# Kernel tuning notes

Measured on AMD Instinct MI355X. Metric: run time of the kernel, lower is better.

## Reference

```python
import jax, jax.numpy as jnp
import numpy as np

NUM_NODES = 16384
NUM_EDGES = 131072
NUM_MOLS = 512
H = 256          # hidden_dim
L = 3            # num_hidden_layers
NUM_RBF = 50
CUTOFF = 5.0
IN_DIM = 5
D_IN = IN_DIM + 3  # atom_types + spherical coords


def setup_inputs() -> dict:
    ks = jax.random.split(jax.random.key(0), 32)
    n = lambda k, s: jax.random.normal(k, s, dtype=jnp.float32) * 0.05
    return {
        "atom_types": jax.random.uniform(ks[0], (NUM_NODES, IN_DIM), dtype=jnp.float32),
        "coords_spherical": jax.random.normal(ks[1], (NUM_NODES, 3), dtype=jnp.float32),
        "edge_dist": jax.random.uniform(ks[2], (NUM_EDGES,), dtype=jnp.float32) * CUTOFF,
        "edge_index": jax.random.randint(ks[3], (2, NUM_EDGES), 0, NUM_NODES, dtype=jnp.int32),
        "node2mol": jnp.arange(NUM_NODES, dtype=jnp.int32) // (NUM_NODES // NUM_MOLS),
        "emb_Wm": n(ks[4], (D_IN, H)), "emb_bm": jnp.zeros((H,), jnp.float32),
        "emb_Wp": n(ks[5], (D_IN, H)), "emb_bp": jnp.zeros((H,), jnp.float32),
        "attn_Wqm": n(ks[6], (L, H, H)), "attn_Wkm": n(ks[7], (L, H, H)), "attn_Wvm": n(ks[8], (L, H, H)),
        "attn_Wqp": n(ks[9], (L, H, H)), "attn_Wkp": n(ks[10], (L, H, H)), "attn_Wvp": n(ks[11], (L, H, H)),
        "attn_We": n(ks[12], (L, NUM_RBF)), "attn_be": jnp.zeros((L,), jnp.float32),
        "mp_We": n(ks[13], (L, NUM_RBF, H)), "mp_be": jnp.zeros((L, H), jnp.float32),
        "mp_Wm": n(ks[14], (L, H, H)), "mp_bm": jnp.zeros((L, H), jnp.float32),
        "mp_Wp": n(ks[15], (L, H, H)), "mp_bp": jnp.zeros((L, H), jnp.float32),
        "ln_g": jnp.ones((L, H), jnp.float32), "ln_b": jnp.zeros((L, H), jnp.float32),
        "proj_W": n(ks[16], (H, H)), "proj_b": jnp.zeros((H,), jnp.float32),
        "head_W1": n(ks[17], (2 * H, H)), "head_b1": jnp.zeros((H,), jnp.float32),
        "head_W2": n(ks[18], (H, H // 2)), "head_b2": jnp.zeros((H // 2,), jnp.float32),
        "head_W3": n(ks[19], (H // 2, 1)), "head_b3": jnp.zeros((1,), jnp.float32),
    }


def _seg_softmax(s, seg, n):
    m = jax.ops.segment_max(s, seg, num_segments=n)
    e = jnp.exp(s - m[seg])
    z = jax.ops.segment_sum(e, seg, num_segments=n)
    return e / (z[seg] + 1e-9)


def _layernorm(x, g, b):
    mu = x.mean(-1, keepdims=True)
    v = ((x - mu) ** 2).mean(-1, keepdims=True)
    return (x - mu) * jax.lax.rsqrt(v + 1e-5) * g + b


def _forward(atom_types, coords_spherical, edge_dist,
             emb_Wm, emb_bm, emb_Wp, emb_bp,
             attn_Wqm, attn_Wkm, attn_Wvm, attn_Wqp, attn_Wkp, attn_Wvp, attn_We, attn_be,
             mp_We, mp_be, mp_Wm, mp_bm, mp_Wp, mp_bp,
             ln_g, ln_b, proj_W, proj_b,
             head_W1, head_b1, head_W2, head_b2, head_W3, head_b3,
             edge_index, node2mol):
    src, dst = edge_index[0], edge_index[1]
    N = NUM_NODES

    # --- RBF expansion (Schutt 2018): 50 gaussians on [0, cutoff] * cosine cutoff ---
    centers = jnp.linspace(0.0, CUTOFF, NUM_RBF)
    delta = CUTOFF / NUM_RBF
    env = 0.5 * (jnp.cos(jnp.pi * edge_dist / CUTOFF) + 1.0) * (edge_dist < CUTOFF)
    rbf = jnp.exp(-0.5 * ((edge_dist[:, None] - centers) / delta) ** 2) * env[:, None]  # [E, R]

    # --- Complex polar embedding ---
    x = jnp.concatenate([atom_types, coords_spherical], axis=-1)  # [N, 8]
    mag = jax.nn.softplus(x @ emb_Wm + emb_bm)
    ph = jnp.pi * jnp.tanh(x @ emb_Wp + emb_bp)

    for l in range(L):
        # --- Complex polar attention: |q||k| cos(phi_q - phi_k), edge bias from rbf ---
        qm, km, vm = mag @ attn_Wqm[l], mag @ attn_Wkm[l], mag @ attn_Wvm[l]
        qp, kp, vp = ph @ attn_Wqp[l], ph @ attn_Wkp[l], ph @ attn_Wvp[l]
        score = jnp.sum(qm[dst] * km[src] * jnp.cos(qp[dst] - kp[src]), axis=-1) / jnp.sqrt(float(H))
        score = score + rbf @ attn_We[l] + attn_be[l]          # [E]
        alpha = _seg_softmax(score, dst, N)                    # [E]
        new_mag = jax.ops.segment_sum(alpha[:, None] * vm[src], dst, num_segments=N)
        new_ph = jax.ops.segment_sum(alpha[:, None] * vp[src], dst, num_segments=N)

        # --- Complex message passing gated by RBF profile ---
        gate = jax.nn.silu(rbf @ mp_We[l] + mp_be[l])          # [E, H]
        agg_m = jax.ops.segment_sum(gate * new_mag[src], dst, num_segments=N)
        agg_p = jax.ops.segment_sum(gate * new_ph[src], dst, num_segments=N)
        new_mag = new_mag + agg_m @ mp_Wm[l] + mp_bm[l]
        new_ph = new_ph + agg_p @ mp_Wp[l] + mp_bp[l]

        # --- residual + LayerNorm on magnitude (dropout = identity at eval) ---
        new_mag = new_mag + mag
        new_ph = new_ph + ph
        mag = _layernorm(new_mag, ln_g[l], ln_b[l])
        ph = new_ph

    # --- real projection + dual (mean, sum) pooling per molecule ---
    atom_repr = (mag * jnp.cos(ph)) @ proj_W + proj_b          # [N, H]
    s = jax.ops.segment_sum(atom_repr, node2mol, num_segments=NUM_MOLS)
    cnt = jax.ops.segment_sum(jnp.ones((N, 1), atom_repr.dtype), node2mol, num_segments=NUM_MOLS)
    mol = jnp.concatenate([s / jnp.maximum(cnt, 1.0), s], axis=-1)  # [B, 2H]

    h = jax.nn.silu(mol @ head_W1 + head_b1)
    h = jax.nn.silu(h @ head_W2 + head_b2)
    return h @ head_W3 + head_b3                               # [B, 1]


def reference(atom_types, coords_spherical, edge_dist,
              emb_Wm, emb_bm, emb_Wp, emb_bp,
              attn_Wqm, attn_Wkm, attn_Wvm, attn_Wqp, attn_Wkp, attn_Wvp, attn_We, attn_be,
              mp_We, mp_be, mp_Wm, mp_bm, mp_Wp, mp_bp,
              ln_g, ln_b, proj_W, proj_b,
              head_W1, head_b1, head_W2, head_b2, head_W3, head_b3,
              edge_index, node2mol):
    return _forward(atom_types, coords_spherical, edge_dist,
                    emb_Wm, emb_bm, emb_Wp, emb_bp,
                    attn_Wqm, attn_Wkm, attn_Wvm, attn_Wqp, attn_Wkp, attn_Wvp, attn_We, attn_be,
                    mp_We, mp_be, mp_Wm, mp_bm, mp_Wp, mp_bp,
                    ln_g, ln_b, proj_W, proj_b,
                    head_W1, head_b1, head_W2, head_b2, head_W3, head_b3,
                    edge_index, node2mol)
```

## Files before the change

kernel.cpp:

```cpp
#include <hip/hip_runtime.h>
#include <math.h>

#define N_NODES 16384
#define N_EDGES 131072
#define N_MOLS 512
#define HDIM 256
#define NLAYER 3
#define NRBF 50
#define CUT 5.0f
#define HH (HDIM*HDIM)

typedef unsigned short u16;
typedef __attribute__((ext_vector_type(8))) short short8v;
typedef __attribute__((ext_vector_type(4))) float f32x4;
typedef __attribute__((ext_vector_type(4))) unsigned short u16x4;
typedef __attribute__((ext_vector_type(8))) unsigned short u16x8;
typedef __attribute__((ext_vector_type(2))) unsigned short u16x2;

__device__ __forceinline__ float softplusf(float x){ return fmaxf(x,0.f)+log1pf(expf(-fabsf(x))); }
__device__ __forceinline__ float siluf(float x){ return x/(1.f+expf(-x)); }
__device__ __forceinline__ float bf2f(u16 u){ union{unsigned int i; float f;}v; v.i=((unsigned int)u)<<16; return v.f; }
__device__ __forceinline__ u16 f2bf(float f){ union{float f; unsigned int i;}v; v.f=f; unsigned int r = v.i + 0x7FFFu + ((v.i>>16)&1u); return (u16)(r>>16); }

__device__ __forceinline__ void gload_lds16(const void* g, void* l){
  __builtin_amdgcn_global_load_lds((const __attribute__((address_space(1))) unsigned int*)g,
                                   (__attribute__((address_space(3))) unsigned int*)l, 16, 0, 0);
}

__global__ void k_hist(const int* __restrict__ dst, int* __restrict__ cnt){
  int e = blockIdx.x*256 + threadIdx.x;
  if(e < N_EDGES) atomicAdd(&cnt[dst[e]], 1);
}

__global__ __launch_bounds__(1024) void k_scan(const int* __restrict__ cnt,
                                               int* __restrict__ rowptr,
                                               int* __restrict__ cursor){
  __shared__ int part[1024];
  int tid = threadIdx.x;
  int base = tid*16;
  int loc[16]; int s=0;
  #pragma unroll
  for(int i=0;i<16;i++){ loc[i]=s; s+=cnt[base+i]; }
  part[tid]=s; __syncthreads();
  for(int off=1; off<1024; off<<=1){
    int v = (tid>=off)? part[tid-off] : 0;
    __syncthreads();
    part[tid] += v;
    __syncthreads();
  }
  int pre = (tid==0)?0:part[tid-1];
  #pragma unroll
  for(int i=0;i<16;i++){ int v = pre+loc[i]; rowptr[base+i]=v; cursor[base+i]=v; }
  if(tid==1023) rowptr[N_NODES]=part[1023];
}

__global__ void k_scatter(const int* __restrict__ dst, const int* __restrict__ src,
                          int* __restrict__ cursor,
                          int* __restrict__ perm, int* __restrict__ srcp){
  int e = blockIdx.x*256+threadIdx.x;
  if(e<N_EDGES){
    int p = atomicAdd(&cursor[dst[e]],1);
    perm[p]=e;
    srcp[p]=src[e];
  }
}

__global__ void k_rbf(const float* __restrict__ dist, const int* __restrict__ perm,
                      u16* __restrict__ rbfp){
  int gid = blockIdx.x*256+threadIdx.x;
  int i = gid>>6, r = gid&63;
  int e = perm[i];
  u16 o = 0;
  if(r<NRBF){
    float d = dist[e];
    float env = 0.5f*(cosf(3.14159265358979f*d/CUT)+1.f) * (d<CUT ? 1.f:0.f);
    float c = CUT*(float)r/(float)(NRBF-1);
    float u = (d - c)/(CUT/(float)NRBF);
    o = f2bf(expf(-0.5f*u*u)*env);
  }
  rbfp[(size_t)i*64+r] = o;
}

struct WDesc { const float* src; u16* dst; int K; int dK; };
struct WArgs { WDesc d[28]; };
__global__ __launch_bounds__(256) void k_wconv(WArgs a){
  WDesc w = a.d[blockIdx.x];
  int t = blockIdx.y;
  int ky = t >> 3, nx = t & 7;
  if(ky*32 >= w.dK) return;
  __shared__ float tile[32][33];
  int tid = threadIdx.x;
  int kk = tid >> 3, n4 = (tid & 7)*4;
  int k = ky*32 + kk;
  float4 v = {0.f,0.f,0.f,0.f};
  if(k < w.K) v = *(const float4*)(w.src + (size_t)k*HDIM + nx*32 + n4);
  tile[kk][n4+0]=v.x; tile[kk][n4+1]=v.y; tile[kk][n4+2]=v.z; tile[kk][n4+3]=v.w;
  __syncthreads();
  int nn = tid >> 3, k4 = (tid & 7)*4;
  u16x4 o;
  #pragma unroll
  for(int j=0;j<4;j++) o[j] = f2bf(tile[k4+j][nn]);
  *(u16x4*)(w.dst + (size_t)(nx*32+nn)*w.dK + ky*32 + k4) = o;
}

__global__ void k_embed(const float* __restrict__ at, const float* __restrict__ co,
                        const float* __restrict__ Wm, const float* __restrict__ bm,
                        const float* __restrict__ Wp, const float* __restrict__ bp,
                        float* __restrict__ mag, float* __restrict__ ph,
                        u16* __restrict__ magb, u16* __restrict__ phb){
  int n = blockIdx.x; int h = threadIdx.x;
  __shared__ float x[8];
  if(threadIdx.x<5) x[threadIdx.x] = at[n*5+threadIdx.x];
  else if(threadIdx.x<8) x[threadIdx.x] = co[n*3+threadIdx.x-5];
  __syncthreads();
  float tm=bm[h], tp=bp[h];
  #pragma unroll
  for(int i=0;i<8;i++){ tm = fmaf(x[i],Wm[i*HDIM+h],tm); tp = fmaf(x[i],Wp[i*HDIM+h],tp); }
  size_t idx = (size_t)n*HDIM+h;
  float m = softplusf(tm);
  float p = 3.14159265358979f*tanhf(tp);
  mag[idx]=m; ph[idx]=p; magb[idx]=f2bf(m); phb[idx]=f2bf(p);
}

template<int MODE>
__device__ __forceinline__ void gemm_fullN(const u16* __restrict__ A,
                                           const u16* __restrict__ Bt,
                                           const float* __restrict__ bias,
                                           void* __restrict__ outp, int K){
  __shared__ __align__(16) u16 As[128*64];
  __shared__ __align__(16) u16 Bs[256*64];
  int tid = threadIdx.x;
  int lane = tid & 63, wid = tid >> 6;
  int wm = wid & 1, wn = wid >> 1;
  int m0 = blockIdx.y * 128;
  const size_t Kb = (size_t)K*2;
  f32x4 acc[4][4] = {};
  for(int k0=0;k0<K;k0+=64){
    #pragma unroll
    for(int it=0; it<2; it++){
      int ci = it*512 + tid;
      int row = ci>>3, cl = ci&7;
      int csw = cl ^ (row&7);
      size_t go = (size_t)(m0+row)*Kb + (size_t)k0*2 + csw*16;
      gload_lds16((const char*)A+go, (char*)As + it*8192 + wid*1024);
    }
    #pragma unroll
    for(int it=0; it<4; it++){
      int ci = it*512 + tid;
      int row = ci>>3, cl = ci&7;
      int csw = cl ^ (row&7);
      size_t go = (size_t)row*Kb + (size_t)k0*2 + csw*16;
      gload_lds16((const char*)Bt+go, (char*)Bs + it*8192 + wid*1024);
    }
    __syncthreads();
    #pragma unroll
    for(int ks=0;ks<2;ks++){
      short8v a[4], b[4];
      #pragma unroll
      for(int fm=0;fm<4;fm++){
        int m = wm*64 + fm*16 + (lane&15);
        int ch = (ks*4 + (lane>>4)) ^ (m&7);
        a[fm] = *(const short8v*)&As[m*64 + ch*8];
      }
      #pragma unroll
      for(int fn=0;fn<4;fn++){
        int n = wn*64 + fn*16 + (lane&15);
        int ch = (ks*4 + (lane>>4)) ^ (n&7);
        b[fn] = *(const short8v*)&Bs[n*64 + ch*8];
      }
      #pragma unroll
      for(int fm=0;fm<4;fm++)
        #pragma unroll
        for(int fn=0;fn<4;fn++)
          acc[fm][fn] = __builtin_amdgcn_mfma_f32_16x16x32_bf16(a[fm], b[fn], acc[fm][fn],0,0,0);
    }
    __syncthreads();
  }
  int ro=(lane>>4)*4, co=lane&15;
  #pragma unroll
  for(int fm=0;fm<4;fm++){
    #pragma unroll
    for(int fn=0;fn<4;fn++){
      int col = wn*64 + fn*16 + co;
      float bv = bias ? bias[col] : 0.f;
      #pragma unroll
      for(int r=0;r<4;r++){
        int row = m0 + wm*64 + fm*16 + ro + r;
        float v = acc[fm][fn][r] + bv;
        size_t ci = (size_t)row*256 + col;
        if(MODE==1) ((u16*)outp)[ci] = f2bf(siluf(v));
        else if(MODE==2) ((float*)outp)[ci] += v;
        else ((float*)outp)[ci] = v;
      }
    }
  }
}

__global__ __launch_bounds__(512) void k_gemm_gate(const u16* __restrict__ rbfp,
                                                   const u16* __restrict__ Wt,
                                                   const float* __restrict__ be,
                                                   u16* __restrict__ gate){
  gemm_fullN<1>(rbfp, Wt, be, gate, 64);
}
struct MpArgs { const u16* A[2]; const u16* Wt[2]; const float* b[2]; float* C[2]; };
__global__ __launch_bounds__(512) void k_gemm_mp(MpArgs a){
  int z = blockIdx.z;
  gemm_fullN<2>(a.A[z], a.Wt[z], a.b[z], a.C[z], HDIM);
}
__global__ __launch_bounds__(512) void k_gemm_proj(const u16* __restrict__ Ab,
                                                   const u16* __restrict__ Wt,
                                                   const float* __restrict__ b,
                                                   float* __restrict__ C){
  gemm_fullN<3>(Ab, Wt, b, C, HDIM);
}

struct Qkv3Args { const u16* Wm[3]; const u16* Wp[3]; u16* qpk; u16* kvpk; };
__global__ __launch_bounds__(512) void k_gemm_qkv3(const u16* __restrict__ magb,
                                                   const u16* __restrict__ phb,
                                                   Qkv3Args a){
  __shared__ __align__(16) u16 Ams[128*64];
  __shared__ __align__(16) u16 Aps[128*64];
  __shared__ __align__(16) u16 Bms[256*64];
  __shared__ __align__(16) u16 Bps[256*64];
  int z = blockIdx.z;
  const u16* Wmz = a.Wm[z];
  const u16* Wpz = a.Wp[z];
  int tid = threadIdx.x;
  int lane = tid & 63, wid = tid >> 6;
  int wm = wid & 1, wn = wid >> 1;
  int m0 = blockIdx.y * 128;
  const size_t Kb = 512;
  f32x4 accm[4][4] = {}, accp[4][4] = {};
  for(int k0=0;k0<256;k0+=64){
    #pragma unroll
    for(int it=0; it<2; it++){
      int ci = it*512 + tid;
      int row = ci>>3, cl = ci&7;
      int csw = cl ^ (row&7);
      size_t go = (size_t)(m0+row)*Kb + (size_t)k0*2 + csw*16;
      gload_lds16((const char*)magb+go, (char*)Ams + it*8192 + wid*1024);
      gload_lds16((const char*)phb +go, (char*)Aps + it*8192 + wid*1024);
    }
    #pragma unroll
    for(int it=0; it<4; it++){
      int ci = it*512 + tid;
      int row = ci>>3, cl = ci&7;
      int csw = cl ^ (row&7);
      size_t go = (size_t)row*Kb + (size_t)k0*2 + csw*16;
      gload_lds16((const char*)Wmz+go, (char*)Bms + it*8192 + wid*1024);
      gload_lds16((const char*)Wpz+go, (char*)Bps + it*8192 + wid*1024);
    }
    __syncthreads();
    #pragma unroll
    for(int ks=0;ks<2;ks++){
      short8v am[4], ap[4], bm_[4], bp_[4];
      #pragma unroll
      for(int fm=0;fm<4;fm++){
        int m = wm*64 + fm*16 + (lane&15);
        int ch = (ks*4 + (lane>>4)) ^ (m&7);
        am[fm] = *(const short8v*)&Ams[m*64 + ch*8];
        ap[fm] = *(const short8v*)&Aps[m*64 + ch*8];
      }
      #pragma unroll
      for(int fn=0;fn<4;fn++){
        int n = wn*64 + fn*16 + (lane&15);
        int ch = (ks*4 + (lane>>4)) ^ (n&7);
        bm_[fn] = *(const short8v*)&Bms[n*64 + ch*8];
        bp_[fn] = *(const short8v*)&Bps[n*64 + ch*8];
      }
      #pragma unroll
      for(int fm=0;fm<4;fm++)
        #pragma unroll
        for(int fn=0;fn<4;fn++){
          accm[fm][fn] = __builtin_amdgcn_mfma_f32_16x16x32_bf16(am[fm], bm_[fn], accm[fm][fn],0,0,0);
          accp[fm][fn] = __builtin_amdgcn_mfma_f32_16x16x32_bf16(ap[fm], bp_[fn], accp[fm][fn],0,0,0);
        }
    }
    __syncthreads();
  }
  int ro=(lane>>4)*4, co=lane&15;
  #pragma unroll
  for(int fm=0;fm<4;fm++){
    #pragma unroll
    for(int fn=0;fn<4;fn++){
      int col = wn*64 + fn*16 + co;
      #pragma unroll
      for(int r=0;r<4;r++){
        int row = m0 + wm*64 + fm*16 + ro + r;
        float mv = accm[fm][fn][r];
        float pv = accp[fm][fn][r];
        u16 o0, o1;
        if(z<2){
          float sn, cs;
          __sincosf(pv, &sn, &cs);
          o0 = f2bf(mv*cs); o1 = f2bf(mv*sn);
        } else {
          o0 = f2bf(mv); o1 = f2bf(pv);
        }
        u16* base = (z==0) ? (a.qpk + (size_t)row*512)
                           : (a.kvpk + (size_t)row*1024 + (z==2 ? 512 : 0));
        base[col] = o0;
        base[col+256] = o1;
      }
    }
  }
}

__global__ __launch_bounds__(256) void k_attn_fused(
    const int* __restrict__ rowptr, const int* __restrict__ srcp,
    const u16* __restrict__ qpack, const u16* __restrict__ kvpack,
    const u16* __restrict__ rbfp,
    const float* __restrict__ We, const float* __restrict__ be,
    float* __restrict__ nmag, float* __restrict__ nph,
    u16* __restrict__ npack)
{
  int wid = threadIdx.x >> 6, lane = threadIdx.x & 63;
  int hid = lane >> 5, l = lane & 31;
  int d = blockIdx.x*4 + wid;
  int b = rowptr[d], e = rowptr[d+1];
  const u16* qb = qpack + (size_t)d*512 + l*8;
  u16x8 qc8 = *(const u16x8*)qb;
  u16x8 qs8 = *(const u16x8*)(qb + 256);
  float qcf[8], qsf[8];
  #pragma unroll
  for(int j=0;j<8;j++){ qcf[j]=bf2f(qc8[j]); qsf[j]=bf2f(qs8[j]); }
  float We0 = (2*l   < NRBF) ? We[2*l]   : 0.f;
  float We1 = (2*l+1 < NRBF) ? We[2*l+1] : 0.f;
  float be0 = be[0];
  float z = 0.f;
  float avm[8] = {0,0,0,0,0,0,0,0}, avp[8] = {0,0,0,0,0,0,0,0};
  for(int i = b + hid; i < e; i += 2){
    int s = srcp[i];
    const u16* kb = kvpack + (size_t)s*1024 + l*8;
    u16x8 kc8 = *(const u16x8*)kb;
    u16x8 ks8 = *(const u16x8*)(kb + 256);
    u16x8 vm8 = *(const u16x8*)(kb + 512);
    u16x8 vp8 = *(const u16x8*)(kb + 768);
    u16x2 rb2 = *(const u16x2*)(rbfp + (size_t)i*64 + 2*l);
    float p = 0.f;
    #pragma unroll
    for(int j=0;j<8;j++){
      p = fmaf(qcf[j], bf2f(kc8[j]), p);
      p = fmaf(qsf[j], bf2f(ks8[j]), p);
    }
    float t = fmaf(bf2f(rb2[0]), We0, fmaf(bf2f(rb2[1]), We1, p*0.0625f));
    #pragma unroll
    for(int off=16; off; off>>=1) t += __shfl_xor(t, off, 64);
    float w = __expf(t + be0);
    z += w;
    #pragma unroll
    for(int j=0;j<8;j++){
      avm[j] = fmaf(w, bf2f(vm8[j]), avm[j]);
      avp[j] = fmaf(w, bf2f(vp8[j]), avp[j]);
    }
  }
  z += __shfl_xor(z, 32, 64);
  #pragma unroll
  for(int j=0;j<8;j++){
    avm[j] += __shfl_xor(avm[j], 32, 64);
    avp[j] += __shfl_xor(avp[j], 32, 64);
  }
  if(hid==0){
    float inv = 1.f/(z + 1e-9f);
    u16x8 mb, pb;
    #pragma unroll
    for(int j=0;j<8;j++){ avm[j]*=inv; avp[j]*=inv; mb[j]=f2bf(avm[j]); pb[j]=f2bf(avp[j]); }
    size_t no = (size_t)d*256 + l*8;
    *(float4*)(nmag + no)     = make_float4(avm[0],avm[1],avm[2],avm[3]);
    *(float4*)(nmag + no + 4) = make_float4(avm[4],avm[5],avm[6],avm[7]);
    *(float4*)(nph + no)      = make_float4(avp[0],avp[1],avp[2],avp[3]);
    *(float4*)(nph + no + 4)  = make_float4(avp[4],avp[5],avp[6],avp[7]);
    u16* nb = npack + (size_t)d*512 + l*8;
    *(u16x8*)nb = mb;
    *(u16x8*)(nb + 256) = pb;
  }
}

__global__ __launch_bounds__(256) void k_mp_agg(const int* __restrict__ rowptr,
                         const int* __restrict__ srcp, const u16* __restrict__ gate,
                         const u16* __restrict__ npack,
                         u16* __restrict__ aggm, u16* __restrict__ aggp){
  int wid = threadIdx.x >> 6, lane = threadIdx.x & 63;
  int hid = lane >> 5, l = lane & 31;
  int n = blockIdx.x*4 + wid;
  int b = rowptr[n], e = rowptr[n+1];
  float am[8] = {0,0,0,0,0,0,0,0}, ap[8] = {0,0,0,0,0,0,0,0};
  for(int i = b + hid; i < e; i += 2){
    int s = srcp[i];
    u16x8 g8 = *(const u16x8*)(gate + (size_t)i*256 + l*8);
    const u16* nb = npack + (size_t)s*512 + l*8;
    u16x8 m8 = *(const u16x8*)nb;
    u16x8 p8 = *(const u16x8*)(nb + 256);
    #pragma unroll
    for(int j=0;j<8;j++){
      float g = bf2f(g8[j]);
      am[j] = fmaf(g, bf2f(m8[j]), am[j]);
      ap[j] = fmaf(g, bf2f(p8[j]), ap[j]);
    }
  }
  #pragma unroll
  for(int j=0;j<8;j++){
    am[j] += __shfl_xor(am[j], 32, 64);
    ap[j] += __shfl_xor(ap[j], 32, 64);
  }
  if(hid==0){
    u16x8 amb, apb;
    #pragma unroll
    for(int j=0;j<8;j++){ amb[j]=f2bf(am[j]); apb[j]=f2bf(ap[j]); }
    size_t o = (size_t)n*256 + l*8;
    *(u16x8*)(aggm + o) = amb;
    *(u16x8*)(aggp + o) = apb;
  }
}

template<int LAST>
__global__ __launch_bounds__(256) void k_resid_ln(const float* __restrict__ nmag, const float* __restrict__ nph,
                           float* __restrict__ mag, float* __restrict__ ph,
                           u16* __restrict__ magb, u16* __restrict__ phb,
                           u16* __restrict__ tcosb,
                           const float* __restrict__ g, const float* __restrict__ b){
  int n = blockIdx.x, tid = threadIdx.x;
  size_t idx = (size_t)n*HDIM+tid;
  float t = nmag[idx] + mag[idx];
  float s1=t, s2=t*t;
  #pragma unroll
  for(int off=32; off; off>>=1){ s1 += __shfl_down(s1,off,64); s2 += __shfl_down(s2,off,64); }
  __shared__ float w1[4], w2[4], bc[2];
  int wid = tid>>6, lane = tid&63;
  if(lane==0){ w1[wid]=s1; w2[wid]=s2; }
  __syncthreads();
  if(tid==0){
    float a=w1[0]+w1[1]+w1[2]+w1[3];
    float q=w2[0]+w2[1]+w2[2]+w2[3];
    float mu = a*(1.f/HDIM);
    float var = q*(1.f/HDIM) - mu*mu;
    bc[0]=mu; bc[1]=rsqrtf(var+1e-5f);
  }
  __syncthreads();
  float mu=bc[0], rs=bc[1];
  float ln = (t-mu)*rs*g[tid]+b[tid];
  float p2 = nph[idx] + ph[idx];
  if(LAST){
    tcosb[idx] = f2bf(ln*__cosf(p2));
  } else {
    mag[idx] = ln; magb[idx] = f2bf(ln);
    ph[idx] = p2; phb[idx] = f2bf(p2);
  }
}

__global__ void k_pool(const float* __restrict__ arepr, const int* __restrict__ n2m,
                       float* __restrict__ spool, float* __restrict__ cntf){
  int gid = blockIdx.x*256+threadIdx.x;
  int n = gid>>8, h = gid&255;
  int m = n2m[n];
  atomicAdd(&spool[(size_t)m*HDIM+h], arepr[(size_t)n*HDIM+h]);
  if(h==0) atomicAdd(&cntf[m], 1.f);
}

__global__ __launch_bounds__(256) void k_head(const float* __restrict__ spool, const float* __restrict__ cntf,
                       const float* __restrict__ W1, const float* __restrict__ b1,
                       const float* __restrict__ W2, const float* __restrict__ b2,
                       const float* __restrict__ W3, const float* __restrict__ b3,
                       float* __restrict__ out){
  __shared__ float smol[2*HDIM];
  __shared__ float sh1[HDIM];
  __shared__ float sh2[HDIM/2];
  int m = blockIdx.x, tid = threadIdx.x;
  float sv = spool[(size_t)m*HDIM+tid];
  float c = cntf[m];
  smol[tid] = sv/fmaxf(c,1.f);
  smol[HDIM+tid] = sv;
  __syncthreads();
  float a = b1[tid];
  for(int i=0;i<2*HDIM;i++) a = fmaf(smol[i], W1[i*HDIM+tid], a);
  sh1[tid] = siluf(a);
  __syncthreads();
  if(tid<128){
    float a2 = b2[tid];
    for(int i=0;i<HDIM;i++) a2 = fmaf(sh1[i], W2[i*128+tid], a2);
    sh2[tid] = siluf(a2);
  }
  __syncthreads();
  if(tid<64){
    float p = sh2[tid]*W3[tid] + sh2[tid+64]*W3[tid+64];
    #pragma unroll
    for(int off=32; off; off>>=1) p += __shfl_down(p,off,64);
    if(tid==0) out[m] = p + b3[0];
  }
}

extern "C" void kernel_launch(void* const* d_in, const int* in_sizes, int n_in,
                              void* d_out, int out_size, void* d_ws, size_t ws_size,
                              hipStream_t stream){
  const float* atom_types = (const float*)d_in[0];
  const float* coords     = (const float*)d_in[1];
  const float* edge_dist  = (const float*)d_in[2];
  const int*   edge_index = (const int*)d_in[3];
  const int*   node2mol   = (const int*)d_in[4];
  const float* emb_Wm = (const float*)d_in[5];
  const float* emb_bm = (const float*)d_in[6];
  const float* emb_Wp = (const float*)d_in[7];
  const float* emb_bp = (const float*)d_in[8];
  const float* attn_Wqm = (const float*)d_in[9];
  const float* attn_Wkm = (const float*)d_in[10];
  const float* attn_Wvm = (const float*)d_in[11];
  const float* attn_Wqp = (const float*)d_in[12];
  const float* attn_Wkp = (const float*)d_in[13];
  const float* attn_Wvp = (const float*)d_in[14];
  const float* attn_We  = (const float*)d_in[15];
  const float* attn_be  = (const float*)d_in[16];
  const float* mp_We = (const float*)d_in[17];
  const float* mp_be = (const float*)d_in[18];
  const float* mp_Wm = (const float*)d_in[19];
  const float* mp_bm = (const float*)d_in[20];
  const float* mp_Wp = (const float*)d_in[21];
  const float* mp_bp = (const float*)d_in[22];
  const float* ln_g = (const float*)d_in[23];
  const float* ln_b = (const float*)d_in[24];
  const float* proj_W = (const float*)d_in[25];
  const float* proj_b = (const float*)d_in[26];
  const float* head_W1 = (const float*)d_in[27];
  const float* head_b1 = (const float*)d_in[28];
  const float* head_W2 = (const float*)d_in[29];
  const float* head_b2 = (const float*)d_in[30];
  const float* head_W3 = (const float*)d_in[31];
  const float* head_b3 = (const float*)d_in[32];
  float* out = (float*)d_out;

  float* ws = (float*)d_ws;
  const size_t NH = (size_t)N_NODES*HDIM;
  size_t o = 0;
  float* mag = ws + o; o += NH;
  float* ph  = ws + o; o += NH;
  float* nmag= ws + o; o += NH;
  float* nph = ws + o; o += NH;
  float* spool = ws + o; o += (size_t)N_MOLS*HDIM;
  float* cntf  = ws + o; o += N_MOLS;
  int* rowptr = (int*)(ws + o); o += N_NODES+1;
  int* cnt    = (int*)(ws + o); o += N_NODES;
  int* cursor = (int*)(ws + o); o += N_NODES;
  int* perm   = (int*)(ws + o); o += N_EDGES;
  int* srcp   = (int*)(ws + o); o += N_EDGES + 1;
  u16* magb = (u16*)(ws + o); o += NH/2;
  u16* phb  = (u16*)(ws + o); o += NH/2;
  u16* aggmb= (u16*)(ws + o); o += NH/2;
  u16* aggpb= (u16*)(ws + o); o += NH/2;
  u16* npack= (u16*)(ws + o); o += NH;
  u16* rbfp = (u16*)(ws + o); o += (size_t)N_EDGES*32;
  u16* qpack= (u16*)(ws + o); o += NH;
  u16* kvpack=(u16*)(ws + o); o += 2*NH;
  o += NH;
  u16* wt   = (u16*)(ws + o); o += (25*(size_t)HH + 3*HDIM*64)/2;
  u16* gatep = qpack;
  float* arepr = nmag;
  u16* tcosb = aggmb;

  const int* src = edge_index;
  const int* dst = edge_index + N_EDGES;

  WArgs wa;
  for(int l=0;l<NLAYER;l++){
    const float* srcs[6] = {attn_Wqm+(size_t)l*HH, attn_Wkm+(size_t)l*HH, attn_Wvm+(size_t)l*HH,
                            attn_Wqp+(size_t)l*HH, attn_Wkp+(size_t)l*HH, attn_Wvp+(size_t)l*HH};
    for(int j=0;j<6;j++){ wa.d[l*6+j] = { srcs[j], wt + (size_t)(l*6+j)*HH, HDIM, HDIM }; }
    wa.d[18+l] = { mp_Wm+(size_t)l*HH, wt + (size_t)(18+l)*HH, HDIM, HDIM };
    wa.d[21+l] = { mp_Wp+(size_t)l*HH, wt + (size_t)(21+l)*HH, HDIM, HDIM };
    wa.d[25+l] = { mp_We+(size_t)l*NRBF*HDIM, wt + (size_t)25*HH + (size_t)l*HDIM*64, NRBF, 64 };
  }
  wa.d[24] = { proj_W, wt + (size_t)24*HH, HDIM, HDIM };

  hipMemsetAsync(cnt, 0, N_NODES*sizeof(int), stream);
  k_hist<<<N_EDGES/256,256,0,stream>>>(dst, cnt);
  k_scan<<<1,1024,0,stream>>>(cnt, rowptr, cursor);
  k_scatter<<<N_EDGES/256,256,0,stream>>>(dst, src, cursor, perm, srcp);
  k_wconv<<<dim3(28,64),256,0,stream>>>(wa);
  k_rbf<<<(N_EDGES*64)/256,256,0,stream>>>(edge_dist, perm, rbfp);
  k_embed<<<N_NODES,256,0,stream>>>(atom_types, coords, emb_Wm, emb_bm, emb_Wp, emb_bp,
                                    mag, ph, magb, phb);

  for(int l=0;l<NLAYER;l++){
    Qkv3Args qa;
    qa.Wm[0] = wt + (size_t)(l*6+0)*HH;
    qa.Wm[1] = wt + (size_t)(l*6+1)*HH;
    qa.Wm[2] = wt + (size_t)(l*6+2)*HH;
    qa.Wp[0] = wt + (size_t)(l*6+3)*HH;
    qa.Wp[1] = wt + (size_t)(l*6+4)*HH;
    qa.Wp[2] = wt + (size_t)(l*6+5)*HH;
    qa.qpk = qpack; qa.kvpk = kvpack;
    k_gemm_qkv3<<<dim3(1,N_NODES/128,3),512,0,stream>>>(magb, phb, qa);
    k_attn_fused<<<N_NODES/4,256,0,stream>>>(rowptr, srcp, qpack, kvpack,
                                             rbfp, attn_We+(size_t)l*NRBF, attn_be+l,
                                             nmag, nph, npack);
    k_gemm_gate<<<dim3(1,N_EDGES/128),512,0,stream>>>(rbfp, wt + (size_t)25*HH + (size_t)l*HDIM*64,
                                                      mp_be+(size_t)l*HDIM, gatep);
    k_mp_agg<<<N_NODES/4,256,0,stream>>>(rowptr, srcp, gatep, npack, aggmb, aggpb);
    MpArgs ma;
    ma.A[0]=aggmb; ma.A[1]=aggpb;
    ma.Wt[0]=wt + (size_t)(18+l)*HH; ma.Wt[1]=wt + (size_t)(21+l)*HH;
    ma.b[0]=mp_bm+(size_t)l*HDIM; ma.b[1]=mp_bp+(size_t)l*HDIM;
    ma.C[0]=nmag; ma.C[1]=nph;
    k_gemm_mp<<<dim3(1,N_NODES/128,2),512,0,stream>>>(ma);
    if(l < NLAYER-1)
      k_resid_ln<0><<<N_NODES,256,0,stream>>>(nmag, nph, mag, ph, magb, phb, nullptr,
                                              ln_g+(size_t)l*HDIM, ln_b+(size_t)l*HDIM);
    else
      k_resid_ln<1><<<N_NODES,256,0,stream>>>(nmag, nph, mag, ph, magb, phb, tcosb,
                                              ln_g+(size_t)l*HDIM, ln_b+(size_t)l*HDIM);
  }
  k_gemm_proj<<<dim3(1,N_NODES/128),512,0,stream>>>(tcosb, wt + (size_t)24*HH, proj_b, arepr);
  hipMemsetAsync(spool, 0, ((size_t)N_MOLS*HDIM+N_MOLS)*sizeof(float), stream);
  k_pool<<<NH/256,256,0,stream>>>(arepr, node2mol, spool, cntf);
  k_head<<<N_MOLS,256,0,stream>>>(spool, cntf, head_W1, head_b1, head_W2, head_b2, head_W3, head_b3, out);
}
```

Baseline: 855.1 us.

## Drop fp32 attention outputs and widen edge-parallel gather lanes to 16 features

The attention kernel no longer writes fp32 nmag/nph. The message-passing GEMM epilogue now adds the bf16 attention output from npack instead of accumulating into the fp32 buffers, which removes a large fp32 write and a read-modify-write. Both gather kernels switch from 2 edges x 32 lanes x 8 features to 4 edges x 16 lanes x 16 features per wave, adding memory-level parallelism at the cost of more registers and an extra shuffle stage. The residual now carries bf16 rounding of the attention output, which slightly changes numerics.

```diff
diff --git a/kernel.cpp b/kernel.cpp
--- a/kernel.cpp
+++ b/kernel.cpp
@@ -15,7 +15,6 @@
 typedef __attribute__((ext_vector_type(4))) float f32x4;
 typedef __attribute__((ext_vector_type(4))) unsigned short u16x4;
 typedef __attribute__((ext_vector_type(8))) unsigned short u16x8;
-typedef __attribute__((ext_vector_type(2))) unsigned short u16x2;
 
 __device__ __forceinline__ float softplusf(float x){ return fmaxf(x,0.f)+log1pf(expf(-fabsf(x))); }
 __device__ __forceinline__ float siluf(float x){ return x/(1.f+expf(-x)); }
@@ -126,7 +125,8 @@
 __device__ __forceinline__ void gemm_fullN(const u16* __restrict__ A,
                                            const u16* __restrict__ Bt,
                                            const float* __restrict__ bias,
-                                           void* __restrict__ outp, int K){
+                                           void* __restrict__ outp, int K,
+                                           const u16* __restrict__ add=nullptr, int aoff=0){
   __shared__ __align__(16) u16 As[128*64];
   __shared__ __align__(16) u16 Bs[256*64];
   int tid = threadIdx.x;
@@ -189,7 +189,7 @@
         float v = acc[fm][fn][r] + bv;
         size_t ci = (size_t)row*256 + col;
         if(MODE==1) ((u16*)outp)[ci] = f2bf(siluf(v));
-        else if(MODE==2) ((float*)outp)[ci] += v;
+        else if(MODE==4) ((float*)outp)[ci] = v + bf2f(add[(size_t)row*512 + aoff + col]);
         else ((float*)outp)[ci] = v;
       }
     }
@@ -202,10 +202,10 @@
                                                    u16* __restrict__ gate){
   gemm_fullN<1>(rbfp, Wt, be, gate, 64);
 }
-struct MpArgs { const u16* A[2]; const u16* Wt[2]; const float* b[2]; float* C[2]; };
+struct MpArgs { const u16* A[2]; const u16* Wt[2]; const float* b[2]; float* C[2]; const u16* add; };
 __global__ __launch_bounds__(512) void k_gemm_mp(MpArgs a){
   int z = blockIdx.z;
-  gemm_fullN<2>(a.A[z], a.Wt[z], a.b[z], a.C[z], HDIM);
+  gemm_fullN<4>(a.A[z], a.Wt[z], a.b[z], a.C[z], HDIM, a.add, z==0?0:256);
 }
 __global__ __launch_bounds__(512) void k_gemm_proj(const u16* __restrict__ Ab,
                                                    const u16* __restrict__ Wt,
@@ -311,68 +311,86 @@
     const u16* __restrict__ qpack, const u16* __restrict__ kvpack,
     const u16* __restrict__ rbfp,
     const float* __restrict__ We, const float* __restrict__ be,
-    float* __restrict__ nmag, float* __restrict__ nph,
     u16* __restrict__ npack)
 {
   int wid = threadIdx.x >> 6, lane = threadIdx.x & 63;
-  int hid = lane >> 5, l = lane & 31;
+  int gid = lane >> 4, l = lane & 15;
   int d = blockIdx.x*4 + wid;
   int b = rowptr[d], e = rowptr[d+1];
-  const u16* qb = qpack + (size_t)d*512 + l*8;
-  u16x8 qc8 = *(const u16x8*)qb;
-  u16x8 qs8 = *(const u16x8*)(qb + 256);
-  float qcf[8], qsf[8];
-  #pragma unroll
-  for(int j=0;j<8;j++){ qcf[j]=bf2f(qc8[j]); qsf[j]=bf2f(qs8[j]); }
-  float We0 = (2*l   < NRBF) ? We[2*l]   : 0.f;
-  float We1 = (2*l+1 < NRBF) ? We[2*l+1] : 0.f;
+  const u16* qb = qpack + (size_t)d*512 + l*16;
+  u16x8 qc0 = *(const u16x8*)qb;
+  u16x8 qc1 = *(const u16x8*)(qb+8);
+  u16x8 qs0 = *(const u16x8*)(qb+256);
+  u16x8 qs1 = *(const u16x8*)(qb+264);
+  float qcf[16], qsf[16];
+  #pragma unroll
+  for(int j=0;j<8;j++){
+    qcf[j]=bf2f(qc0[j]); qcf[j+8]=bf2f(qc1[j]);
+    qsf[j]=bf2f(qs0[j]); qsf[j+8]=bf2f(qs1[j]);
+  }
+  float Wef[4];
+  #pragma unroll
+  for(int k=0;k<4;k++) Wef[k] = (l*4+k < NRBF) ? We[l*4+k] : 0.f;
   float be0 = be[0];
   float z = 0.f;
-  float avm[8] = {0,0,0,0,0,0,0,0}, avp[8] = {0,0,0,0,0,0,0,0};
-  for(int i = b + hid; i < e; i += 2){
+  float avm[16], avp[16];
+  #pragma unroll
+  for(int j=0;j<16;j++){ avm[j]=0.f; avp[j]=0.f; }
+  for(int i = b + gid; i < e; i += 4){
     int s = srcp[i];
-    const u16* kb = kvpack + (size_t)s*1024 + l*8;
-    u16x8 kc8 = *(const u16x8*)kb;
-    u16x8 ks8 = *(const u16x8*)(kb + 256);
-    u16x8 vm8 = *(const u16x8*)(kb + 512);
-    u16x8 vp8 = *(const u16x8*)(kb + 768);
-    u16x2 rb2 = *(const u16x2*)(rbfp + (size_t)i*64 + 2*l);
+    const u16* kb = kvpack + (size_t)s*1024 + l*16;
+    u16x8 kc0 = *(const u16x8*)kb;
+    u16x8 kc1 = *(const u16x8*)(kb+8);
+    u16x8 ks0 = *(const u16x8*)(kb+256);
+    u16x8 ks1 = *(const u16x8*)(kb+264);
+    u16x8 vm0 = *(const u16x8*)(kb+512);
+    u16x8 vm1 = *(const u16x8*)(kb+520);
+    u16x8 vp0 = *(const u16x8*)(kb+768);
+    u16x8 vp1 = *(const u16x8*)(kb+776);
+    u16x4 rb4 = *(const u16x4*)(rbfp + (size_t)i*64 + l*4);
     float p = 0.f;
     #pragma unroll
     for(int j=0;j<8;j++){
-      p = fmaf(qcf[j], bf2f(kc8[j]), p);
-      p = fmaf(qsf[j], bf2f(ks8[j]), p);
-    }
-    float t = fmaf(bf2f(rb2[0]), We0, fmaf(bf2f(rb2[1]), We1, p*0.0625f));
-    #pragma unroll
-    for(int off=16; off; off>>=1) t += __shfl_xor(t, off, 64);
+      p = fmaf(qcf[j],   bf2f(kc0[j]), p);
+      p = fmaf(qcf[j+8], bf2f(kc1[j]), p);
+      p = fmaf(qsf[j],   bf2f(ks0[j]), p);
+      p = fmaf(qsf[j+8], bf2f(ks1[j]), p);
+    }
+    float t = p*0.0625f;
+    #pragma unroll
+    for(int k=0;k<4;k++) t = fmaf(bf2f(rb4[k]), Wef[k], t);
+    #pragma unroll
+    for(int off=8; off; off>>=1) t += __shfl_xor(t, off, 64);
     float w = __expf(t + be0);
     z += w;
     #pragma unroll
     for(int j=0;j<8;j++){
-      avm[j] = fmaf(w, bf2f(vm8[j]), avm[j]);
-      avp[j] = fmaf(w, bf2f(vp8[j]), avp[j]);
-    }
-  }
+      avm[j]   = fmaf(w, bf2f(vm0[j]), avm[j]);
+      avm[j+8] = fmaf(w, bf2f(vm1[j]), avm[j+8]);
+      avp[j]   = fmaf(w, bf2f(vp0[j]), avp[j]);
+      avp[j+8] = fmaf(w, bf2f(vp1[j]), avp[j+8]);
+    }
+  }
+  z += __shfl_xor(z, 16, 64);
   z += __shfl_xor(z, 32, 64);
   #pragma unroll
-  for(int j=0;j<8;j++){
+  for(int j=0;j<16;j++){
+    avm[j] += __shfl_xor(avm[j], 16, 64);
     avm[j] += __shfl_xor(avm[j], 32, 64);
+    avp[j] += __shfl_xor(avp[j], 16, 64);
     avp[j] += __shfl_xor(avp[j], 32, 64);
   }
-  if(hid==0){
+  if(gid==0){
     float inv = 1.f/(z + 1e-9f);
-    u16x8 mb, pb;
-    #pragma unroll
-    for(int j=0;j<8;j++){ avm[j]*=inv; avp[j]*=inv; mb[j]=f2bf(avm[j]); pb[j]=f2bf(avp[j]); }
-    size_t no = (size_t)d*256 + l*8;
-    *(float4*)(nmag + no)     = make_float4(avm[0],avm[1],avm[2],avm[3]);
-    *(float4*)(nmag + no + 4) = make_float4(avm[4],avm[5],avm[6],avm[7]);
-    *(float4*)(nph + no)      = make_float4(avp[0],avp[1],avp[2],avp[3]);
-    *(float4*)(nph + no + 4)  = make_float4(avp[4],avp[5],avp[6],avp[7]);
-    u16* nb = npack + (size_t)d*512 + l*8;
-    *(u16x8*)nb = mb;
-    *(u16x8*)(nb + 256) = pb;
+    u16x8 m0, m1, p0, p1;
+    #pragma unroll
+    for(int j=0;j<8;j++){
+      m0[j]=f2bf(avm[j]*inv); m1[j]=f2bf(avm[j+8]*inv);
+      p0[j]=f2bf(avp[j]*inv); p1[j]=f2bf(avp[j+8]*inv);
+    }
+    u16* nb = npack + (size_t)d*512 + l*16;
+    *(u16x8*)nb = m0;       *(u16x8*)(nb+8)   = m1;
+    *(u16x8*)(nb+256) = p0; *(u16x8*)(nb+264) = p1;
   }
 }
 
@@ -381,35 +399,48 @@
                          const u16* __restrict__ npack,
                          u16* __restrict__ aggm, u16* __restrict__ aggp){
   int wid = threadIdx.x >> 6, lane = threadIdx.x & 63;
-  int hid = lane >> 5, l = lane & 31;
+  int gid = lane >> 4, l = lane & 15;
   int n = blockIdx.x*4 + wid;
   int b = rowptr[n], e = rowptr[n+1];
-  float am[8] = {0,0,0,0,0,0,0,0}, ap[8] = {0,0,0,0,0,0,0,0};
-  for(int i = b + hid; i < e; i += 2){
+  float am[16], ap[16];
+  #pragma unroll
+  for(int j=0;j<16;j++){ am[j]=0.f; ap[j]=0.f; }
+  for(int i = b + gid; i < e; i += 4){
     int s = srcp[i];
-    u16x8 g8 = *(const u16x8*)(gate + (size_t)i*256 + l*8);
-    const u16* nb = npack + (size_t)s*512 + l*8;
-    u16x8 m8 = *(const u16x8*)nb;
-    u16x8 p8 = *(const u16x8*)(nb + 256);
+    const u16* gb = gate + (size_t)i*256 + l*16;
+    u16x8 g0 = *(const u16x8*)gb;
+    u16x8 g1 = *(const u16x8*)(gb+8);
+    const u16* nb = npack + (size_t)s*512 + l*16;
+    u16x8 m0 = *(const u16x8*)nb;
+    u16x8 m1 = *(const u16x8*)(nb+8);
+    u16x8 p0 = *(const u16x8*)(nb+256);
+    u16x8 p1 = *(const u16x8*)(nb+264);
     #pragma unroll
     for(int j=0;j<8;j++){
-      float g = bf2f(g8[j]);
-      am[j] = fmaf(g, bf2f(m8[j]), am[j]);
-      ap[j] = fmaf(g, bf2f(p8[j]), ap[j]);
-    }
-  }
-  #pragma unroll
-  for(int j=0;j<8;j++){
+      float ga = bf2f(g0[j]), gb2 = bf2f(g1[j]);
+      am[j]   = fmaf(ga,  bf2f(m0[j]), am[j]);
+      am[j+8] = fmaf(gb2, bf2f(m1[j]), am[j+8]);
+      ap[j]   = fmaf(ga,  bf2f(p0[j]), ap[j]);
+      ap[j+8] = fmaf(gb2, bf2f(p1[j]), ap[j+8]);
+    }
+  }
+  #pragma unroll
+  for(int j=0;j<16;j++){
+    am[j] += __shfl_xor(am[j], 16, 64);
     am[j] += __shfl_xor(am[j], 32, 64);
+    ap[j] += __shfl_xor(ap[j], 16, 64);
     ap[j] += __shfl_xor(ap[j], 32, 64);
   }
-  if(hid==0){
-    u16x8 amb, apb;
-    #pragma unroll
-    for(int j=0;j<8;j++){ amb[j]=f2bf(am[j]); apb[j]=f2bf(ap[j]); }
-    size_t o = (size_t)n*256 + l*8;
-    *(u16x8*)(aggm + o) = amb;
-    *(u16x8*)(aggp + o) = apb;
+  if(gid==0){
+    u16x8 a0, a1, b0, b1;
+    #pragma unroll
+    for(int j=0;j<8;j++){
+      a0[j]=f2bf(am[j]); a1[j]=f2bf(am[j+8]);
+      b0[j]=f2bf(ap[j]); b1[j]=f2bf(ap[j+8]);
+    }
+    size_t o = (size_t)n*256 + l*16;
+    *(u16x8*)(aggm + o) = a0; *(u16x8*)(aggm + o + 8) = a1;
+    *(u16x8*)(aggp + o) = b0; *(u16x8*)(aggp + o + 8) = b1;
   }
 }
 
@@ -590,7 +621,7 @@
     k_gemm_qkv3<<<dim3(1,N_NODES/128,3),512,0,stream>>>(magb, phb, qa);
     k_attn_fused<<<N_NODES/4,256,0,stream>>>(rowptr, srcp, qpack, kvpack,
                                              rbfp, attn_We+(size_t)l*NRBF, attn_be+l,
-                                             nmag, nph, npack);
+                                             npack);
     k_gemm_gate<<<dim3(1,N_EDGES/128),512,0,stream>>>(rbfp, wt + (size_t)25*HH + (size_t)l*HDIM*64,
                                                       mp_be+(size_t)l*HDIM, gatep);
     k_mp_agg<<<N_NODES/4,256,0,stream>>>(rowptr, srcp, gatep, npack, aggmb, aggpb);
@@ -599,6 +630,7 @@
     ma.Wt[0]=wt + (size_t)(18+l)*HH; ma.Wt[1]=wt + (size_t)(21+l)*HH;
     ma.b[0]=mp_bm+(size_t)l*HDIM; ma.b[1]=mp_bp+(size_t)l*HDIM;
     ma.C[0]=nmag; ma.C[1]=nph;
+    ma.add = npack;
     k_gemm_mp<<<dim3(1,N_NODES/128,2),512,0,stream>>>(ma);
     if(l < NLAYER-1)
       k_resid_ln<0><<<N_NODES,256,0,stream>>>(nmag, nph, mag, ph, magb, phb, nullptr,
```

Measured after the change: 857.6 us. About the same (+0.3%).
